# Optimization experiments

Hardware: AMD Instinct MI355X
Metric: run time of the kernel (lower is better)

Reference implementation:

```python
import jax, jax.numpy as jnp
import numpy as np

G = 500          # num graphs
NODES_PER_G = 1000
EDGES_PER_G = 2000
N = G * NODES_PER_G   # 500_000 total nodes
E = G * EDGES_PER_G   # 1_000_000 total edges
DN, DE, DG, DO = 128, 64, 128, 128


def setup_inputs() -> dict:
    key = jax.random.key(0)
    ks = jax.random.split(key, 7)
    return {
        "node_features": jax.random.normal(ks[0], (N, DN), dtype=jnp.float32),
        "edge_features": jax.random.normal(ks[1], (E, DE), dtype=jnp.float32),
        "global_features": jax.random.normal(ks[2], (G, DG), dtype=jnp.float32),
        "W_node": jax.random.normal(ks[3], (DO, DN), dtype=jnp.float32) / np.sqrt(DN),
        "W_edges": jax.random.normal(ks[4], (DO, DE), dtype=jnp.float32) / np.sqrt(DE),
        "W_global": jax.random.normal(ks[5], (DO, DG), dtype=jnp.float32) / np.sqrt(DG),
        "bias": jax.random.normal(ks[6], (DO,), dtype=jnp.float32) * 0.01,
        "num_nodes_by_graph": jnp.full((G,), NODES_PER_G, dtype=jnp.int32),
        "num_edges_by_graph": jnp.full((G,), EDGES_PER_G, dtype=jnp.int32),
    }


def _segment_mean(feats, lengths, num_segments, total):
    # segment ids from per-graph lengths (segment_lengths_to_ids)
    ids = jnp.repeat(jnp.arange(num_segments, dtype=jnp.int32), lengths,
                     total_repeat_length=total)
    s = jax.ops.segment_sum(feats, ids, num_segments=num_segments)
    cnt = jnp.maximum(lengths, 1).astype(feats.dtype)[:, None]
    return s / cnt


def reference(node_features, edge_features, global_features,
              W_node, W_edges, W_global, bias,
              num_nodes_by_graph, num_edges_by_graph):
    # mean-aggregate nodes/edges per graph, then linear projections summed
    node_agg = _segment_mean(node_features, num_nodes_by_graph, G, N)   # [G, DN]
    edge_agg = _segment_mean(edge_features, num_edges_by_graph, G, E)   # [G, DE]
    out = (jnp.einsum('gd,od->go', node_agg, W_node)
           + jnp.einsum('gd,od->go', edge_agg, W_edges)
           + jnp.einsum('gd,od->go', global_features, W_global)
           + bias)
    return out
```

## Files before the change

### kernel.cpp

```cpp
#include <hip/hip_runtime.h>
#include <stdint.h>


#define DN 128
#define DE 64
#define DO 128
#define NCHUNK 4
#define NW 4
#define SLOTS 8

template<int N> __device__ __forceinline__ void wait_vmcnt() {
    __builtin_amdgcn_s_waitcnt(0x0F70 | (N & 0xF) | ((N >> 4) << 14));
    __asm__ volatile("" ::: "memory");
}

__global__ __launch_bounds__(512) void scan_offsets_kernel(
    const int* __restrict__ nlen, const int* __restrict__ elen, int G,
    int* __restrict__ noff, int* __restrict__ eoff)
{
    __shared__ int sn[512], se[512];
    __shared__ int carry_n, carry_e;
    const int t = threadIdx.x;
    if (t == 0) { carry_n = 0; carry_e = 0; }
    __syncthreads();

    for (int base = 0; base < G; base += 512) {
        const int idx = base + t;
        const int vn = (idx < G) ? nlen[idx] : 0;
        const int ve = (idx < G) ? elen[idx] : 0;
        sn[t] = vn; se[t] = ve;
        __syncthreads();
        for (int off = 1; off < 512; off <<= 1) {
            const int an = (t >= off) ? sn[t - off] : 0;
            const int ae = (t >= off) ? se[t - off] : 0;
            __syncthreads();
            sn[t] += an; se[t] += ae;
            __syncthreads();
        }
        if (idx < G) {
            noff[idx] = carry_n + sn[t] - vn;
            eoff[idx] = carry_e + se[t] - ve;
        }
        __syncthreads();
        if (t == 0) {
            const int last = (G - base < 512) ? (G - base - 1) : 511;
            carry_n += sn[last];
            carry_e += se[last];
        }
        __syncthreads();
    }
}

__global__ __launch_bounds__(256) void agg_kernel(
    const float* __restrict__ nodes, const float* __restrict__ edges,
    const int* __restrict__ noff, const int* __restrict__ eoff,
    const int* __restrict__ nlen, const int* __restrict__ elen,
    float* __restrict__ nsum, float* __restrict__ esum, int G)
{
    __shared__ float4 ring[NW * SLOTS * 64];
    const int b = blockIdx.x;
    const int t = threadIdx.x;
    const int lane = t & 63;
    const int w = t >> 6;

    const bool is_node = (b < G * NCHUNK);
    const int gb = is_node ? b : (b - G * NCHUNK);
    const int g = gb / NCHUNK;
    const int c = gb % NCHUNK;
    const int RF = is_node ? (DN / 4) : (DE / 4);
    const int len = is_node ? nlen[g] : elen[g];
    const int off = is_node ? noff[g] : eoff[g];
    const float4* __restrict__ src4 =
        (const float4*)(is_node ? nodes : edges);
    float* __restrict__ dst =
        is_node ? &nsum[(size_t)g * DN] : &esum[(size_t)g * DE];

    const size_t fbase = (size_t)off * RF;
    const int span_total = len * RF;
    const int chunk = ((span_total + NCHUNK * 64 - 1) / (NCHUNK * 64)) * 64;
    const int fs = c * chunk;
    int fe = fs + chunk; if (fe > span_total) fe = span_total;
    const int span = (fe > fs) ? (fe - fs) : 0;
    const int nslots = span >> 6;
    const int rem = span & 63;

    const int ns_w = (nslots > w) ? ((nslots - w + NW - 1) / NW) : 0;

    char* ringc = (char*)ring;

    auto issue = [&](int k) {
        const int s = w + k * NW;
        const float4* gp = src4 + fbase + (size_t)fs + (size_t)s * 64 + lane;
        __builtin_amdgcn_global_load_lds(
            (const __attribute__((address_space(1))) void*)gp,
            (__attribute__((address_space(3))) void*)
                (ringc + (((w * SLOTS) + (k % SLOTS)) << 10)),
            16, 0, 0);
    };
    float4 acc = make_float4(0.f, 0.f, 0.f, 0.f);
    auto consume = [&](int k) {
        const float4* sp =
            (const float4*)(ringc + (((w * SLOTS) + (k % SLOTS)) << 10));
        const float4 v = sp[lane];
        acc.x += v.x; acc.y += v.y; acc.z += v.z; acc.w += v.w;
    };

    const int pre = (ns_w < SLOTS) ? ns_w : SLOTS;
    for (int k = 0; k < pre; ++k) issue(k);

    int k = 0;
    for (; k + SLOTS < ns_w; ++k) {
        wait_vmcnt<SLOTS - 1>();
        consume(k);
        issue(k + SLOTS);
    }
    {
        const int m = ns_w - k;
        if (m > 7) { wait_vmcnt<7>(); consume(ns_w - 8); }
        if (m > 6) { wait_vmcnt<6>(); consume(ns_w - 7); }
        if (m > 5) { wait_vmcnt<5>(); consume(ns_w - 6); }
        if (m > 4) { wait_vmcnt<4>(); consume(ns_w - 5); }
        if (m > 3) { wait_vmcnt<3>(); consume(ns_w - 4); }
        if (m > 2) { wait_vmcnt<2>(); consume(ns_w - 3); }
        if (m > 1) { wait_vmcnt<1>(); consume(ns_w - 2); }
        if (m > 0) { wait_vmcnt<0>(); consume(ns_w - 1); }
    }

    if (rem && t < rem) {
        const int f = fs + (nslots << 6) + t;
        const float4 v = src4[fbase + f];
        const int col = f & (RF - 1);
        atomicAdd(&dst[col * 4 + 0], v.x);
        atomicAdd(&dst[col * 4 + 1], v.y);
        atomicAdd(&dst[col * 4 + 2], v.z);
        atomicAdd(&dst[col * 4 + 3], v.w);
    }

    __syncthreads();
    float4* sm = ring;
    sm[t] = acc;
    __syncthreads();
    const int tmin = RF;
    for (int sdist = 128; sdist >= tmin; sdist >>= 1) {
        if (t < sdist) {
            const float4 o = sm[t + sdist];
            sm[t].x += o.x; sm[t].y += o.y; sm[t].z += o.z; sm[t].w += o.w;
        }
        __syncthreads();
    }
    if (t < RF) {
        const float4 v = sm[t];
        atomicAdd(&dst[t * 4 + 0], v.x);
        atomicAdd(&dst[t * 4 + 1], v.y);
        atomicAdd(&dst[t * 4 + 2], v.z);
        atomicAdd(&dst[t * 4 + 3], v.w);
    }
}

__global__ __launch_bounds__(128) void finalize_kernel(
    const float* __restrict__ nsum, const float* __restrict__ esum,
    const float* __restrict__ glob,
    const float* __restrict__ Wn, const float* __restrict__ We,
    const float* __restrict__ Wg, const float* __restrict__ bias,
    const int* __restrict__ nlen, const int* __restrict__ elen,
    float* __restrict__ out)
{
    __shared__ float sn[DN], se_[DE], sg[DN];
    const int g = blockIdx.x;
    const int o = threadIdx.x;

    const int nl = nlen[g];
    const int el = elen[g];
    const float inv_n = 1.0f / (float)((nl > 1) ? nl : 1);
    const float inv_e = 1.0f / (float)((el > 1) ? el : 1);

    sn[o] = nsum[(size_t)g * DN + o] * inv_n;
    sg[o] = glob[(size_t)g * DN + o];
    if (o < DE) se_[o] = esum[(size_t)g * DE + o] * inv_e;
    __syncthreads();

    float acc = bias[o];
    const float4* __restrict__ wn = (const float4*)(Wn + (size_t)o * DN);
    const float4* __restrict__ wg = (const float4*)(Wg + (size_t)o * DN);
    const float4* __restrict__ we = (const float4*)(We + (size_t)o * DE);
    const float4* s4n = (const float4*)sn;
    const float4* s4g = (const float4*)sg;
    const float4* s4e = (const float4*)se_;

    #pragma unroll
    for (int i = 0; i < DN / 4; ++i) {
        const float4 a = wn[i], v = s4n[i];
        acc += a.x * v.x + a.y * v.y + a.z * v.z + a.w * v.w;
    }
    #pragma unroll
    for (int i = 0; i < DN / 4; ++i) {
        const float4 a = wg[i], v = s4g[i];
        acc += a.x * v.x + a.y * v.y + a.z * v.z + a.w * v.w;
    }
    #pragma unroll
    for (int i = 0; i < DE / 4; ++i) {
        const float4 a = we[i], v = s4e[i];
        acc += a.x * v.x + a.y * v.y + a.z * v.z + a.w * v.w;
    }
    out[(size_t)g * DO + o] = acc;
}

extern "C" void kernel_launch(void* const* d_in, const int* in_sizes, int n_in,
                              void* d_out, int out_size, void* d_ws, size_t ws_size,
                              hipStream_t stream)
{
    const float* nodes = (const float*)d_in[0];
    const float* edges = (const float*)d_in[1];
    const float* glob  = (const float*)d_in[2];
    const float* Wn    = (const float*)d_in[3];
    const float* We    = (const float*)d_in[4];
    const float* Wg    = (const float*)d_in[5];
    const float* Wg2   = (const float*)d_in[5];
    const float* bias  = (const float*)d_in[6];
    const int*   nlen  = (const int*)d_in[7];
    const int*   elen  = (const int*)d_in[8];
    float*       out   = (float*)d_out;
    (void)Wg2;

    const int G = in_sizes[7];

    float* nsum = (float*)d_ws;
    float* esum = nsum + (size_t)G * DN;
    int*   noff = (int*)(esum + (size_t)G * DE);
    int*   eoff = noff + G;

    hipMemsetAsync(d_ws, 0, (size_t)G * (DN + DE) * sizeof(float), stream);

    scan_offsets_kernel<<<1, 512, 0, stream>>>(nlen, elen, G, noff, eoff);

    const int agg_blocks = G * NCHUNK * 2;
    agg_kernel<<<agg_blocks, 256, 0, stream>>>(nodes, edges, noff, eoff,
                                               nlen, elen, nsum, esum, G);

    finalize_kernel<<<G, 128, 0, stream>>>(nsum, esum, glob, Wn, We, Wg, bias,
                                           nlen, elen, out);
}
```

Baseline: 514.5 us.

## Replace LDS-ring async loads with unrolled nontemporal register loads, double chunks

Drops the global_load_lds ring-buffer pipeline with explicit vmcnt waits. Each wave now streams its contiguous slot range into registers using nontemporal loads, unrolled by four into four independent accumulators. Per-graph chunks go from 4 to 8, so twice as many blocks run and each wave covers a contiguous balanced range. The intent is more memory parallelism and less LDS traffic for this bandwidth-bound reduction, at the cost of more blocks, more atomics and reliance on the compiler keeping enough loads in flight.

Result: faster. 484.0 us (-5.9%).

```diff
diff --git a/kernel.cpp b/kernel.cpp
--- a/kernel.cpp
+++ b/kernel.cpp
@@ -1,17 +1,17 @@
 #include <hip/hip_runtime.h>
-#include <stdint.h>
 
 
 #define DN 128
 #define DE 64
 #define DO 128
-#define NCHUNK 4
+#define NCHUNK 8
 #define NW 4
-#define SLOTS 8
-
-template<int N> __device__ __forceinline__ void wait_vmcnt() {
-    __builtin_amdgcn_s_waitcnt(0x0F70 | (N & 0xF) | ((N >> 4) << 14));
-    __asm__ volatile("" ::: "memory");
+#define U  4
+
+typedef float f4v __attribute__((ext_vector_type(4)));
+
+__device__ __forceinline__ f4v nt_load(const f4v* p) {
+    return __builtin_nontemporal_load(p);
 }
 
 __global__ __launch_bounds__(512) void scan_offsets_kernel(
@@ -57,7 +57,7 @@
     const int* __restrict__ nlen, const int* __restrict__ elen,
     float* __restrict__ nsum, float* __restrict__ esum, int G)
 {
-    __shared__ float4 ring[NW * SLOTS * 64];
+    __shared__ f4v sm[256];
     const int b = blockIdx.x;
     const int t = threadIdx.x;
     const int lane = t & 63;
@@ -70,65 +70,41 @@
     const int RF = is_node ? (DN / 4) : (DE / 4);
     const int len = is_node ? nlen[g] : elen[g];
     const int off = is_node ? noff[g] : eoff[g];
-    const float4* __restrict__ src4 =
-        (const float4*)(is_node ? nodes : edges);
+    const f4v* __restrict__ src =
+        (const f4v*)(is_node ? nodes : edges) + (size_t)off * RF;
     float* __restrict__ dst =
         is_node ? &nsum[(size_t)g * DN] : &esum[(size_t)g * DE];
 
-    const size_t fbase = (size_t)off * RF;
-    const int span_total = len * RF;
-    const int chunk = ((span_total + NCHUNK * 64 - 1) / (NCHUNK * 64)) * 64;
-    const int fs = c * chunk;
-    int fe = fs + chunk; if (fe > span_total) fe = span_total;
-    const int span = (fe > fs) ? (fe - fs) : 0;
-    const int nslots = span >> 6;
-    const int rem = span & 63;
-
-    const int ns_w = (nslots > w) ? ((nslots - w + NW - 1) / NW) : 0;
-
-    char* ringc = (char*)ring;
-
-    auto issue = [&](int k) {
-        const int s = w + k * NW;
-        const float4* gp = src4 + fbase + (size_t)fs + (size_t)s * 64 + lane;
-        __builtin_amdgcn_global_load_lds(
-            (const __attribute__((address_space(1))) void*)gp,
-            (__attribute__((address_space(3))) void*)
-                (ringc + (((w * SLOTS) + (k % SLOTS)) << 10)),
-            16, 0, 0);
-    };
-    float4 acc = make_float4(0.f, 0.f, 0.f, 0.f);
-    auto consume = [&](int k) {
-        const float4* sp =
-            (const float4*)(ringc + (((w * SLOTS) + (k % SLOTS)) << 10));
-        const float4 v = sp[lane];
-        acc.x += v.x; acc.y += v.y; acc.z += v.z; acc.w += v.w;
-    };
-
-    const int pre = (ns_w < SLOTS) ? ns_w : SLOTS;
-    for (int k = 0; k < pre; ++k) issue(k);
-
+    const int T = len * RF;
+    const int nslots = T >> 6;
+    const int rem = T & 63;
+
+    const int per_c = nslots / NCHUNK, ex_c = nslots % NCHUNK;
+    const int cs = c * per_c + (c < ex_c ? c : ex_c);
+    const int cn = per_c + (c < ex_c ? 1 : 0);
+    const int per_w = cn / NW, ex_w = cn % NW;
+    const int ws = cs + w * per_w + (w < ex_w ? w : ex_w);
+    const int wn = per_w + (w < ex_w ? 1 : 0);
+
+    const f4v* __restrict__ p = src + ((size_t)ws << 6) + lane;
+
+    f4v a0 = {0.f, 0.f, 0.f, 0.f}, a1 = a0, a2 = a0, a3 = a0;
     int k = 0;
-    for (; k + SLOTS < ns_w; ++k) {
-        wait_vmcnt<SLOTS - 1>();
-        consume(k);
-        issue(k + SLOTS);
-    }
-    {
-        const int m = ns_w - k;
-        if (m > 7) { wait_vmcnt<7>(); consume(ns_w - 8); }
-        if (m > 6) { wait_vmcnt<6>(); consume(ns_w - 7); }
-        if (m > 5) { wait_vmcnt<5>(); consume(ns_w - 6); }
-        if (m > 4) { wait_vmcnt<4>(); consume(ns_w - 5); }
-        if (m > 3) { wait_vmcnt<3>(); consume(ns_w - 4); }
-        if (m > 2) { wait_vmcnt<2>(); consume(ns_w - 3); }
-        if (m > 1) { wait_vmcnt<1>(); consume(ns_w - 2); }
-        if (m > 0) { wait_vmcnt<0>(); consume(ns_w - 1); }
-    }
-
-    if (rem && t < rem) {
-        const int f = fs + (nslots << 6) + t;
-        const float4 v = src4[fbase + f];
+    for (; k + U <= wn; k += U) {
+        const f4v v0 = nt_load(p + ((size_t)(k + 0) << 6));
+        const f4v v1 = nt_load(p + ((size_t)(k + 1) << 6));
+        const f4v v2 = nt_load(p + ((size_t)(k + 2) << 6));
+        const f4v v3 = nt_load(p + ((size_t)(k + 3) << 6));
+        a0 += v0; a1 += v1; a2 += v2; a3 += v3;
+    }
+    for (; k < wn; ++k) {
+        a0 += nt_load(p + ((size_t)k << 6));
+    }
+    const f4v acc = (a0 + a1) + (a2 + a3);
+
+    if (c == 0 && rem && t < rem) {
+        const int f = (nslots << 6) + t;
+        const f4v v = nt_load(src + f);
         const int col = f & (RF - 1);
         atomicAdd(&dst[col * 4 + 0], v.x);
         atomicAdd(&dst[col * 4 + 1], v.y);
@@ -136,20 +112,14 @@
         atomicAdd(&dst[col * 4 + 3], v.w);
     }
 
-    __syncthreads();
-    float4* sm = ring;
     sm[t] = acc;
     __syncthreads();
-    const int tmin = RF;
-    for (int sdist = 128; sdist >= tmin; sdist >>= 1) {
-        if (t < sdist) {
-            const float4 o = sm[t + sdist];
-            sm[t].x += o.x; sm[t].y += o.y; sm[t].z += o.z; sm[t].w += o.w;
-        }
+    for (int s = 128; s >= RF; s >>= 1) {
+        if (t < s) sm[t] += sm[t + s];
         __syncthreads();
     }
     if (t < RF) {
-        const float4 v = sm[t];
+        const f4v v = sm[t];
         atomicAdd(&dst[t * 4 + 0], v.x);
         atomicAdd(&dst[t * 4 + 1], v.y);
         atomicAdd(&dst[t * 4 + 2], v.z);
@@ -215,12 +185,10 @@
     const float* Wn    = (const float*)d_in[3];
     const float* We    = (const float*)d_in[4];
     const float* Wg    = (const float*)d_in[5];
-    const float* Wg2   = (const float*)d_in[5];
     const float* bias  = (const float*)d_in[6];
     const int*   nlen  = (const int*)d_in[7];
     const int*   elen  = (const int*)d_in[8];
     float*       out   = (float*)d_out;
-    (void)Wg2;
 
     const int G = in_sizes[7];
 
```
